# Kernel optimization log

Measured on AMD Instinct MI355X. Metric: run time of the kernel, lower is better.

## Reference

```python
import jax, jax.numpy as jnp
import numpy as np

N, E = 50000, 800000
NODE_DIM, EDGE_DIM = 96, 64
IN_DIM = 2 * NODE_DIM + EDGE_DIM  # 256


def setup_inputs() -> dict:
    key = jax.random.key(0)
    k = jax.random.split(key, 7)
    h = jax.random.normal(k[0], (N, NODE_DIM), dtype=jnp.float32)
    edge_index = jax.random.randint(k[1], (2, E), 0, N, dtype=jnp.int64)
    edge_attr = jax.random.normal(k[2], (E, EDGE_DIM), dtype=jnp.float32)
    # Linear params (PyTorch default-ish scale)
    s = 1.0 / np.sqrt(IN_DIM)
    W_e = jax.random.uniform(k[3], (IN_DIM, NODE_DIM), jnp.float32, -s, s)
    b_e = jax.random.uniform(k[4], (NODE_DIM,), jnp.float32, -s, s)
    W_n = jax.random.uniform(k[5], (IN_DIM, NODE_DIM), jnp.float32, -s, s)
    b_n = jax.random.uniform(k[6], (NODE_DIM,), jnp.float32, -s, s)
    return {"h": h, "edge_index": edge_index, "edge_attr": edge_attr,
            "W_e": W_e, "b_e": b_e, "W_n": W_n, "b_n": b_n}


def reference(h, edge_index, edge_attr, W_e, b_e, W_n, b_n):
    src, dst = edge_index[0], edge_index[1]
    concat = jnp.concatenate([h[src], h[dst], edge_attr], axis=-1)  # [E, 256]
    gates = jax.nn.sigmoid(concat @ W_e + b_e)                      # [E, node_dim]
    messages = jax.nn.softplus(concat @ W_n + b_n)                  # [E, node_dim]
    gated = gates * messages
    n = h.shape[0]
    h_new = jax.ops.segment_sum(gated, dst, num_segments=n)         # [N, node_dim]
    edge_count = jax.ops.segment_sum(jnp.ones((dst.shape[0],), h.dtype), dst, num_segments=n)
    edge_count = jnp.clip(edge_count, 1.0, None)[:, None]
    return h + h_new / edge_count
```

## Files before the change

kernel.cpp:

```cpp
#include <hip/hip_runtime.h>
#include <hip/hip_bf16.h>


#define NODE_DIM 96
#define EDGE_DIM 64
#define IN_DIM   256
#define NT_TILES 12
#define KT_TILES 8

typedef float  f32x4  __attribute__((ext_vector_type(4)));
typedef __bf16 bf16x8 __attribute__((ext_vector_type(8)));

__device__ __forceinline__ unsigned short bf16rne(float f) {
    unsigned int u = __float_as_uint(f);
    u += 0x7FFFu + ((u >> 16) & 1u);
    return (unsigned short)(u >> 16);
}

__global__ void pack_w_kernel(const float* __restrict__ We,
                              const float* __restrict__ Wn,
                              unsigned short* __restrict__ bpack) {
    int t = blockIdx.x * blockDim.x + threadIdx.x;
    if (t >= KT_TILES * NT_TILES * 64) return;
    int tile = t >> 6, lane = t & 63;
    int kt = tile / NT_TILES, nt = tile % NT_TILES;
    const float* W = (nt < 6) ? We : Wn;
    int n  = (nt % 6) * 16 + (lane & 15);
    int k0 = kt * 32 + (lane >> 4) * 8;
    union { unsigned short u[8]; uint4 v; } tmp;
#pragma unroll
    for (int j = 0; j < 8; ++j) tmp.u[j] = bf16rne(W[(k0 + j) * NODE_DIM + n]);
    *(uint4*)(bpack + (size_t)t * 8) = tmp.v;
}

__global__ void cvt_h_kernel(const float* __restrict__ h,
                             unsigned short* __restrict__ hb, int total8) {
    int i = blockIdx.x * 256 + threadIdx.x;
    if (i >= total8) return;
    const float4 v0 = ((const float4*)h)[i * 2];
    const float4 v1 = ((const float4*)h)[i * 2 + 1];
    union { unsigned short u[8]; uint4 v; } p;
    p.u[0] = bf16rne(v0.x); p.u[1] = bf16rne(v0.y);
    p.u[2] = bf16rne(v0.z); p.u[3] = bf16rne(v0.w);
    p.u[4] = bf16rne(v1.x); p.u[5] = bf16rne(v1.y);
    p.u[6] = bf16rne(v1.z); p.u[7] = bf16rne(v1.w);
    ((uint4*)hb)[i] = p.v;
}

__global__ void hist_kernel(const int* __restrict__ eidx, unsigned* __restrict__ deg, int E) {
    int e = blockIdx.x * 256 + threadIdx.x;
    if (e < E) atomicAdd(deg + eidx[E + e], 1u);
}

__device__ __forceinline__ unsigned block_excl_scan_256(unsigned v, int tid,
                                                        unsigned* wsum, unsigned* wpre,
                                                        unsigned* total) {
    int lane = tid & 63, w = tid >> 6;
    unsigned inc = v;
#pragma unroll
    for (int o = 1; o < 64; o <<= 1) {
        unsigned t = __shfl_up(inc, o, 64);
        if (lane >= o) inc += t;
    }
    if (lane == 63) wsum[w] = inc;
    __syncthreads();
    if (tid == 0) {
        unsigned s = 0;
#pragma unroll
        for (int k = 0; k < 4; ++k) { wpre[k] = s; s += wsum[k]; }
        *total = s;
    }
    __syncthreads();
    return inc - v + wpre[w];
}

__global__ void scan_block_kernel(const unsigned* __restrict__ deg,
                                  unsigned* __restrict__ scanned,
                                  unsigned* __restrict__ blocksum, int N) {
    __shared__ unsigned wsum[4], wpre[4], total;
    int tid = threadIdx.x;
    int i = blockIdx.x * 256 + tid;
    unsigned v = (i < N) ? deg[i] : 0u;
    unsigned excl = block_excl_scan_256(v, tid, wsum, wpre, &total);
    if (i < N) scanned[i] = excl;
    if (tid == 0) blocksum[blockIdx.x] = total;
}

__global__ void scan_sums_kernel(const unsigned* __restrict__ blocksum,
                                 unsigned* __restrict__ blockpref, int NB) {
    __shared__ unsigned wsum[4], wpre[4], total;
    int tid = threadIdx.x;
    unsigned v = (tid < NB) ? blocksum[tid] : 0u;
    unsigned excl = block_excl_scan_256(v, tid, wsum, wpre, &total);
    if (tid < NB) blockpref[tid] = excl;
}

__global__ void scan_finalize_kernel(const unsigned* __restrict__ scanned,
                                     const unsigned* __restrict__ blockpref,
                                     unsigned* __restrict__ offsets,
                                     unsigned* __restrict__ cursor, int N, int E) {
    int i = blockIdx.x * 256 + threadIdx.x;
    if (i < N) {
        unsigned o = scanned[i] + blockpref[i >> 8];
        offsets[i] = o;
        cursor[i]  = o;
    }
    if (i == 0) offsets[N] = (unsigned)E;
}

__global__ void scatter_kernel(const int* __restrict__ eidx,
                               unsigned* __restrict__ cursor,
                               int2* __restrict__ s_se,
                               int*  __restrict__ s_d,
                               int E) {
    int e = blockIdx.x * 256 + threadIdx.x;
    if (e < E) {
        int s = eidx[e];
        int d = eidx[E + e];
        unsigned pos = atomicAdd(cursor + d, 1u);
        s_se[pos] = make_int2(s, e);
        s_d[pos]  = d;
    }
}

__global__ __launch_bounds__(256, 3)
void gemm_sorted_kernel(const unsigned short* __restrict__ hb,
                        const int2* __restrict__ s_se,
                        const int*  __restrict__ s_d,
                        const float* __restrict__ ea,
                        const unsigned short* __restrict__ bpack,
                        const float* __restrict__ be,
                        const float* __restrict__ bn,
                        float* __restrict__ hnew,
                        int E) {
    const int tid  = threadIdx.x;
    const int wave = tid >> 6, lane = tid & 63;
    const int m    = lane & 15;
    const int quad = lane >> 4;
    const int base = blockIdx.x * 128 + wave * 32;

    const unsigned short* hsq[2];
    const unsigned short* hdq[2];
    const float*          epq[2];
    int dstv[2];
#pragma unroll
    for (int mt = 0; mt < 2; ++mt) {
        int r  = base + mt * 16 + m;
        int rg = (r < E) ? r : (E - 1);
        int2 se = s_se[rg];
        int dst = s_d[rg];
        dstv[mt] = dst;
        hsq[mt] = hb + (size_t)se.x * NODE_DIM + quad * 8;
        hdq[mt] = hb + (size_t)dst  * NODE_DIM + quad * 8;
        epq[mt] = ea + (size_t)se.y * EDGE_DIM + quad * 8;
    }
    const unsigned short* bl = bpack + lane * 8;

    f32x4 acc[2][NT_TILES];
#pragma unroll
    for (int mt = 0; mt < 2; ++mt)
#pragma unroll
        for (int nt = 0; nt < NT_TILES; ++nt) acc[mt][nt] = (f32x4){0.f, 0.f, 0.f, 0.f};

#pragma unroll
    for (int kt = 0; kt < KT_TILES; ++kt) {
        bf16x8 A[2];
#pragma unroll
        for (int mt = 0; mt < 2; ++mt) {
            if (kt < 3) {
                A[mt] = *(const bf16x8*)(hsq[mt] + kt * 32);
            } else if (kt < 6) {
                A[mt] = *(const bf16x8*)(hdq[mt] + (kt - 3) * 32);
            } else {
                const float4 v0 = *(const float4*)(epq[mt] + (kt - 6) * 32);
                const float4 v1 = *(const float4*)(epq[mt] + (kt - 6) * 32 + 4);
                union { unsigned short u[8]; bf16x8 b; } t;
                t.u[0] = bf16rne(v0.x); t.u[1] = bf16rne(v0.y);
                t.u[2] = bf16rne(v0.z); t.u[3] = bf16rne(v0.w);
                t.u[4] = bf16rne(v1.x); t.u[5] = bf16rne(v1.y);
                t.u[6] = bf16rne(v1.z); t.u[7] = bf16rne(v1.w);
                A[mt] = t.b;
            }
        }
#pragma unroll
        for (int nt = 0; nt < NT_TILES; ++nt) {
            bf16x8 bfrag = *(const bf16x8*)(bl + (kt * NT_TILES + nt) * 512);
            acc[0][nt] = __builtin_amdgcn_mfma_f32_16x16x32_bf16(A[0], bfrag, acc[0][nt], 0, 0, 0);
            acc[1][nt] = __builtin_amdgcn_mfma_f32_16x16x32_bf16(A[1], bfrag, acc[1][nt], 0, 0, 0);
        }
    }

#pragma unroll
    for (int mt = 0; mt < 2; ++mt) {
        int dprev = -1;
        float s[6];
#pragma unroll
        for (int r = 0; r < 4; ++r) {
            const int ee = base + mt * 16 + quad * 4 + r;
            const int d  = __shfl(dstv[mt], quad * 4 + r, 64);
            if (ee >= E) continue;
            float v[6];
#pragma unroll
            for (int nt = 0; nt < 6; ++nt) {
                const int col = nt * 16 + m;
                float g  = acc[mt][nt][r]     + be[col];
                float mm = acc[mt][nt + 6][r] + bn[col];
                float gate = 1.0f / (1.0f + __expf(-g));
                float sp   = fmaxf(mm, 0.0f) + __logf(1.0f + __expf(-fabsf(mm)));
                v[nt] = gate * sp;
            }
            if (d != dprev) {
                if (dprev >= 0) {
                    float* hrow = hnew + (size_t)dprev * NODE_DIM + m;
#pragma unroll
                    for (int nt = 0; nt < 6; ++nt) unsafeAtomicAdd(hrow + nt * 16, s[nt]);
                }
#pragma unroll
                for (int nt = 0; nt < 6; ++nt) s[nt] = v[nt];
                dprev = d;
            } else {
#pragma unroll
                for (int nt = 0; nt < 6; ++nt) s[nt] += v[nt];
            }
        }
        if (dprev >= 0) {
            float* hrow = hnew + (size_t)dprev * NODE_DIM + m;
#pragma unroll
            for (int nt = 0; nt < 6; ++nt) unsafeAtomicAdd(hrow + nt * 16, s[nt]);
        }
    }
}

__global__ void finalize_kernel(const float* __restrict__ h,
                                const float* __restrict__ hnew,
                                const unsigned* __restrict__ offsets,
                                float* __restrict__ out,
                                int total4) {
    int i = blockIdx.x * blockDim.x + threadIdx.x;
    if (i >= total4) return;
    int n = i / 24;
    unsigned deg = offsets[n + 1] - offsets[n];
    float inv = 1.0f / (float)(deg > 0u ? deg : 1u);
    float4 hv = ((const float4*)h)[i];
    float4 av = ((const float4*)hnew)[i];
    float4 o = {hv.x + av.x * inv, hv.y + av.y * inv, hv.z + av.z * inv, hv.w + av.w * inv};
    ((float4*)out)[i] = o;
}

extern "C" void kernel_launch(void* const* d_in, const int* in_sizes, int n_in,
                              void* d_out, int out_size, void* d_ws, size_t ws_size,
                              hipStream_t stream) {
    const float* h   = (const float*)d_in[0];
    const int*   ei  = (const int*)  d_in[1];
    const float* ea  = (const float*)d_in[2];
    const float* We  = (const float*)d_in[3];
    const float* be  = (const float*)d_in[4];
    const float* Wn  = (const float*)d_in[5];
    const float* bn  = (const float*)d_in[6];

    const int N = in_sizes[0] / NODE_DIM;
    const int E = in_sizes[2] / EDGE_DIM;
    char* ws = (char*)d_ws;

    size_t off = 0;
    auto take = [&](size_t bytes) { size_t o = off; off = (off + bytes + 511) & ~(size_t)511; return o; };
    const size_t O_BPACK = take((size_t)KT_TILES * NT_TILES * 64 * 16);
    const size_t O_DEG   = take((size_t)N * 4);
    const size_t O_HNEW  = take((size_t)N * NODE_DIM * 4);
    const size_t O_MEMSET_END = off;
    const size_t O_SCAN  = take((size_t)N * 4);
    const size_t O_BSUM  = take(1024);
    const size_t O_BPREF = take(1024);
    const size_t O_OFFS  = take((size_t)(N + 1) * 4);
    const size_t O_CURS  = take((size_t)N * 4);
    const size_t O_SSE   = take((size_t)E * 8);
    const size_t O_SD    = take((size_t)E * 4);
    const size_t O_HB    = take((size_t)N * NODE_DIM * 2);
    (void)ws_size;

    unsigned short* bpack = (unsigned short*)(ws + O_BPACK);
    unsigned* deg   = (unsigned*)(ws + O_DEG);
    float*    hnew  = (float*)(ws + O_HNEW);
    unsigned* scn   = (unsigned*)(ws + O_SCAN);
    unsigned* bsum  = (unsigned*)(ws + O_BSUM);
    unsigned* bpref = (unsigned*)(ws + O_BPREF);
    unsigned* offs  = (unsigned*)(ws + O_OFFS);
    unsigned* curs  = (unsigned*)(ws + O_CURS);
    int2*     s_se  = (int2*)(ws + O_SSE);
    int*      s_d   = (int*)(ws + O_SD);
    unsigned short* hb = (unsigned short*)(ws + O_HB);

    hipMemsetAsync(ws + O_DEG, 0, O_MEMSET_END - O_DEG, stream);

    pack_w_kernel<<<(KT_TILES * NT_TILES * 64 + 255) / 256, 256, 0, stream>>>(We, Wn, bpack);

    const int total8 = N * NODE_DIM / 8;
    cvt_h_kernel<<<(total8 + 255) / 256, 256, 0, stream>>>(h, hb, total8);

    const int NB = (N + 255) / 256;
    hist_kernel<<<(E + 255) / 256, 256, 0, stream>>>(ei, deg, E);
    scan_block_kernel<<<NB, 256, 0, stream>>>(deg, scn, bsum, N);
    scan_sums_kernel<<<1, 256, 0, stream>>>(bsum, bpref, NB);
    scan_finalize_kernel<<<NB, 256, 0, stream>>>(scn, bpref, offs, curs, N, E);
    scatter_kernel<<<(E + 255) / 256, 256, 0, stream>>>(ei, curs, s_se, s_d, E);

    gemm_sorted_kernel<<<(E + 127) / 128, 256, 0, stream>>>(hb, s_se, s_d, ea, bpack,
                                                            be, bn, hnew, E);

    const int total4 = N * (NODE_DIM / 4);
    finalize_kernel<<<(total4 + 255) / 256, 256, 0, stream>>>(h, hnew, offs, (float*)d_out, total4);
}
```

Baseline: 645.7 us.

## Fuse setup kernels, single-block scan, pre-sort bf16 edge attrs, two tiles per wave

Merges weight packing, h conversion and the degree histogram into one launch, and replaces the three-kernel scan with a single 1024-thread block scan. The scatter kernel now converts edge_attr to bf16 and writes it in dst-sorted order, so the GEMM reads contiguous bf16 rows instead of gathering fp32 rows by original edge index. The GEMM processes two 32-row tiles per wave, loading all A fragments up front and prefetching the second tile before the first epilogue. Occupancy hint drops from 3 to 2 blocks, and bias values are hoisted into registers. The trade-off is that the single-block scan serialises over N and the scatter kernel takes on extra write traffic.

```diff
diff --git a/kernel.cpp b/kernel.cpp
--- a/kernel.cpp
+++ b/kernel.cpp
@@ -4,9 +4,9 @@
 
 #define NODE_DIM 96
 #define EDGE_DIM 64
-#define IN_DIM   256
 #define NT_TILES 12
 #define KT_TILES 8
+#define PACK_BLOCKS 24
 
 typedef float  f32x4  __attribute__((ext_vector_type(4)));
 typedef __bf16 bf16x8 __attribute__((ext_vector_type(8)));
@@ -17,117 +17,120 @@
     return (unsigned short)(u >> 16);
 }
 
-__global__ void pack_w_kernel(const float* __restrict__ We,
-                              const float* __restrict__ Wn,
-                              unsigned short* __restrict__ bpack) {
-    int t = blockIdx.x * blockDim.x + threadIdx.x;
-    if (t >= KT_TILES * NT_TILES * 64) return;
-    int tile = t >> 6, lane = t & 63;
-    int kt = tile / NT_TILES, nt = tile % NT_TILES;
-    const float* W = (nt < 6) ? We : Wn;
-    int n  = (nt % 6) * 16 + (lane & 15);
-    int k0 = kt * 32 + (lane >> 4) * 8;
-    union { unsigned short u[8]; uint4 v; } tmp;
-#pragma unroll
-    for (int j = 0; j < 8; ++j) tmp.u[j] = bf16rne(W[(k0 + j) * NODE_DIM + n]);
-    *(uint4*)(bpack + (size_t)t * 8) = tmp.v;
-}
-
-__global__ void cvt_h_kernel(const float* __restrict__ h,
-                             unsigned short* __restrict__ hb, int total8) {
-    int i = blockIdx.x * 256 + threadIdx.x;
-    if (i >= total8) return;
-    const float4 v0 = ((const float4*)h)[i * 2];
-    const float4 v1 = ((const float4*)h)[i * 2 + 1];
-    union { unsigned short u[8]; uint4 v; } p;
-    p.u[0] = bf16rne(v0.x); p.u[1] = bf16rne(v0.y);
-    p.u[2] = bf16rne(v0.z); p.u[3] = bf16rne(v0.w);
-    p.u[4] = bf16rne(v1.x); p.u[5] = bf16rne(v1.y);
-    p.u[6] = bf16rne(v1.z); p.u[7] = bf16rne(v1.w);
-    ((uint4*)hb)[i] = p.v;
-}
-
-__global__ void hist_kernel(const int* __restrict__ eidx, unsigned* __restrict__ deg, int E) {
-    int e = blockIdx.x * 256 + threadIdx.x;
-    if (e < E) atomicAdd(deg + eidx[E + e], 1u);
-}
-
-__device__ __forceinline__ unsigned block_excl_scan_256(unsigned v, int tid,
-                                                        unsigned* wsum, unsigned* wpre,
-                                                        unsigned* total) {
-    int lane = tid & 63, w = tid >> 6;
-    unsigned inc = v;
-#pragma unroll
-    for (int o = 1; o < 64; o <<= 1) {
-        unsigned t = __shfl_up(inc, o, 64);
-        if (lane >= o) inc += t;
+__global__ __launch_bounds__(256)
+void setup_kernel(const float* __restrict__ We, const float* __restrict__ Wn,
+                  unsigned short* __restrict__ bpack,
+                  const float* __restrict__ h, unsigned short* __restrict__ hb,
+                  int total8,
+                  const int* __restrict__ eidx, unsigned* __restrict__ deg,
+                  int E, int cvtB) {
+    const int b = blockIdx.x, tid = threadIdx.x;
+    if (b < PACK_BLOCKS) {
+        int t = b * 256 + tid;
+        if (t < KT_TILES * NT_TILES * 64) {
+            int tile = t >> 6, lane = t & 63;
+            int kt = tile / NT_TILES, nt = tile % NT_TILES;
+            const float* W = (nt < 6) ? We : Wn;
+            int n  = (nt % 6) * 16 + (lane & 15);
+            int k0 = kt * 32 + (lane >> 4) * 8;
+            union { unsigned short u[8]; uint4 v; } tmp;
+#pragma unroll
+            for (int j = 0; j < 8; ++j) tmp.u[j] = bf16rne(W[(k0 + j) * NODE_DIM + n]);
+            *(uint4*)(bpack + (size_t)t * 8) = tmp.v;
+        }
+    } else if (b < PACK_BLOCKS + cvtB) {
+        int i = (b - PACK_BLOCKS) * 256 + tid;
+        if (i < total8) {
+            const float4 v0 = ((const float4*)h)[i * 2];
+            const float4 v1 = ((const float4*)h)[i * 2 + 1];
+            union { unsigned short u[8]; uint4 v; } p;
+            p.u[0] = bf16rne(v0.x); p.u[1] = bf16rne(v0.y);
+            p.u[2] = bf16rne(v0.z); p.u[3] = bf16rne(v0.w);
+            p.u[4] = bf16rne(v1.x); p.u[5] = bf16rne(v1.y);
+            p.u[6] = bf16rne(v1.z); p.u[7] = bf16rne(v1.w);
+            ((uint4*)hb)[i] = p.v;
+        }
+    } else {
+        int e = (b - PACK_BLOCKS - cvtB) * 256 + tid;
+        if (e < E) atomicAdd(deg + eidx[E + e], 1u);
     }
-    if (lane == 63) wsum[w] = inc;
-    __syncthreads();
-    if (tid == 0) {
-        unsigned s = 0;
-#pragma unroll
-        for (int k = 0; k < 4; ++k) { wpre[k] = s; s += wsum[k]; }
-        *total = s;
+}
+
+__global__ __launch_bounds__(1024)
+void scan_kernel(const unsigned* __restrict__ deg,
+                 unsigned* __restrict__ offsets,
+                 unsigned* __restrict__ cursor, int N) {
+    __shared__ unsigned lds_w[16], lds_p[16], lds_tot;
+    const int tid = threadIdx.x, lane = tid & 63, wv = tid >> 6;
+    unsigned carry = 0;
+    for (int base = 0; base < N; base += 1024) {
+        int i = base + tid;
+        unsigned v = (i < N) ? deg[i] : 0u;
+        unsigned inc = v;
+#pragma unroll
+        for (int o = 1; o < 64; o <<= 1) {
+            unsigned t = __shfl_up(inc, o, 64);
+            if (lane >= o) inc += t;
+        }
+        if (lane == 63) lds_w[wv] = inc;
+        __syncthreads();
+        if (tid == 0) {
+            unsigned s = 0;
+#pragma unroll
+            for (int k = 0; k < 16; ++k) { unsigned x = lds_w[k]; lds_p[k] = s; s += x; }
+            lds_tot = s;
+        }
+        __syncthreads();
+        unsigned excl = inc - v + lds_p[wv] + carry;
+        if (i < N) { offsets[i] = excl; cursor[i] = excl; }
+        carry += lds_tot;
+        __syncthreads();
     }
-    __syncthreads();
-    return inc - v + wpre[w];
-}
-
-__global__ void scan_block_kernel(const unsigned* __restrict__ deg,
-                                  unsigned* __restrict__ scanned,
-                                  unsigned* __restrict__ blocksum, int N) {
-    __shared__ unsigned wsum[4], wpre[4], total;
-    int tid = threadIdx.x;
-    int i = blockIdx.x * 256 + tid;
-    unsigned v = (i < N) ? deg[i] : 0u;
-    unsigned excl = block_excl_scan_256(v, tid, wsum, wpre, &total);
-    if (i < N) scanned[i] = excl;
-    if (tid == 0) blocksum[blockIdx.x] = total;
-}
-
-__global__ void scan_sums_kernel(const unsigned* __restrict__ blocksum,
-                                 unsigned* __restrict__ blockpref, int NB) {
-    __shared__ unsigned wsum[4], wpre[4], total;
-    int tid = threadIdx.x;
-    unsigned v = (tid < NB) ? blocksum[tid] : 0u;
-    unsigned excl = block_excl_scan_256(v, tid, wsum, wpre, &total);
-    if (tid < NB) blockpref[tid] = excl;
-}
-
-__global__ void scan_finalize_kernel(const unsigned* __restrict__ scanned,
-                                     const unsigned* __restrict__ blockpref,
-                                     unsigned* __restrict__ offsets,
-                                     unsigned* __restrict__ cursor, int N, int E) {
-    int i = blockIdx.x * 256 + threadIdx.x;
-    if (i < N) {
-        unsigned o = scanned[i] + blockpref[i >> 8];
-        offsets[i] = o;
-        cursor[i]  = o;
+    if (tid == 0) offsets[N] = carry;
+}
+
+__global__ __launch_bounds__(256)
+void scatter_kernel(const int* __restrict__ eidx, const float* __restrict__ ea,
+                    unsigned* __restrict__ cursor,
+                    int2* __restrict__ s_sd, unsigned short* __restrict__ seab,
+                    int E) {
+    const int tid = threadIdx.x, wave = tid >> 6, lane = tid & 63;
+    const int ebase = blockIdx.x * 256 + wave * 64;
+    const int e = ebase + lane;
+    unsigned pos = 0u;
+    if (e < E) {
+        int s = eidx[e], d = eidx[E + e];
+        pos = atomicAdd(cursor + d, 1u);
+        s_sd[pos] = make_int2(s, d);
     }
-    if (i == 0) offsets[N] = (unsigned)E;
-}
-
-__global__ void scatter_kernel(const int* __restrict__ eidx,
-                               unsigned* __restrict__ cursor,
-                               int2* __restrict__ s_se,
-                               int*  __restrict__ s_d,
-                               int E) {
-    int e = blockIdx.x * 256 + threadIdx.x;
-    if (e < E) {
-        int s = eidx[e];
-        int d = eidx[E + e];
-        unsigned pos = atomicAdd(cursor + d, 1u);
-        s_se[pos] = make_int2(s, e);
-        s_d[pos]  = d;
+#pragma unroll
+    for (int ph = 0; ph < 4; ++ph) {
+        const int el = ph * 16 + (lane >> 2);
+        const int q  = lane & 3;
+        const unsigned p = (unsigned)__shfl((int)pos, el, 64);
+        const int eo = ebase + el;
+        if (eo < E) {
+            const float4* pr = (const float4*)(ea + (size_t)eo * EDGE_DIM) + q * 4;
+            const float4 v0 = pr[0], v1 = pr[1], v2 = pr[2], v3 = pr[3];
+            union { unsigned short u[16]; uint4 v[2]; } t;
+            t.u[0]  = bf16rne(v0.x); t.u[1]  = bf16rne(v0.y);
+            t.u[2]  = bf16rne(v0.z); t.u[3]  = bf16rne(v0.w);
+            t.u[4]  = bf16rne(v1.x); t.u[5]  = bf16rne(v1.y);
+            t.u[6]  = bf16rne(v1.z); t.u[7]  = bf16rne(v1.w);
+            t.u[8]  = bf16rne(v2.x); t.u[9]  = bf16rne(v2.y);
+            t.u[10] = bf16rne(v2.z); t.u[11] = bf16rne(v2.w);
+            t.u[12] = bf16rne(v3.x); t.u[13] = bf16rne(v3.y);
+            t.u[14] = bf16rne(v3.z); t.u[15] = bf16rne(v3.w);
+            uint4* dp = (uint4*)(seab + (size_t)p * EDGE_DIM + q * 16);
+            dp[0] = t.v[0]; dp[1] = t.v[1];
+        }
     }
 }
 
-__global__ __launch_bounds__(256, 3)
+__global__ __launch_bounds__(256, 2)
 void gemm_sorted_kernel(const unsigned short* __restrict__ hb,
-                        const int2* __restrict__ s_se,
-                        const int*  __restrict__ s_d,
-                        const float* __restrict__ ea,
+                        const int2* __restrict__ s_sd,
+                        const unsigned short* __restrict__ seab,
                         const unsigned short* __restrict__ bpack,
                         const float* __restrict__ be,
                         const float* __restrict__ bn,
@@ -137,98 +140,112 @@
     const int wave = tid >> 6, lane = tid & 63;
     const int m    = lane & 15;
     const int quad = lane >> 4;
-    const int base = blockIdx.x * 128 + wave * 32;
-
-    const unsigned short* hsq[2];
-    const unsigned short* hdq[2];
-    const float*          epq[2];
-    int dstv[2];
-#pragma unroll
-    for (int mt = 0; mt < 2; ++mt) {
-        int r  = base + mt * 16 + m;
-        int rg = (r < E) ? r : (E - 1);
-        int2 se = s_se[rg];
-        int dst = s_d[rg];
-        dstv[mt] = dst;
-        hsq[mt] = hb + (size_t)se.x * NODE_DIM + quad * 8;
-        hdq[mt] = hb + (size_t)dst  * NODE_DIM + quad * 8;
-        epq[mt] = ea + (size_t)se.y * EDGE_DIM + quad * 8;
-    }
+    const int wbase = (blockIdx.x * 4 + wave) * 64;
+
     const unsigned short* bl = bpack + lane * 8;
 
+    float bev[6], bnv[6];
+#pragma unroll
+    for (int nt = 0; nt < 6; ++nt) { bev[nt] = be[nt * 16 + m]; bnv[nt] = bn[nt * 16 + m]; }
+
+    int2 sd[2][2];
+#pragma unroll
+    for (int T = 0; T < 2; ++T)
+#pragma unroll
+        for (int mt = 0; mt < 2; ++mt) {
+            int r  = wbase + T * 32 + mt * 16 + m;
+            int rg = (r < E) ? r : (E - 1);
+            sd[T][mt] = s_sd[rg];
+        }
+
+    bf16x8 a[2][8];
     f32x4 acc[2][NT_TILES];
-#pragma unroll
-    for (int mt = 0; mt < 2; ++mt)
-#pragma unroll
-        for (int nt = 0; nt < NT_TILES; ++nt) acc[mt][nt] = (f32x4){0.f, 0.f, 0.f, 0.f};
-
-#pragma unroll
-    for (int kt = 0; kt < KT_TILES; ++kt) {
-        bf16x8 A[2];
+
+    auto load_a = [&](int T) {
 #pragma unroll
         for (int mt = 0; mt < 2; ++mt) {
-            if (kt < 3) {
-                A[mt] = *(const bf16x8*)(hsq[mt] + kt * 32);
-            } else if (kt < 6) {
-                A[mt] = *(const bf16x8*)(hdq[mt] + (kt - 3) * 32);
-            } else {
-                const float4 v0 = *(const float4*)(epq[mt] + (kt - 6) * 32);
-                const float4 v1 = *(const float4*)(epq[mt] + (kt - 6) * 32 + 4);
-                union { unsigned short u[8]; bf16x8 b; } t;
-                t.u[0] = bf16rne(v0.x); t.u[1] = bf16rne(v0.y);
-                t.u[2] = bf16rne(v0.z); t.u[3] = bf16rne(v0.w);
-                t.u[4] = bf16rne(v1.x); t.u[5] = bf16rne(v1.y);
-                t.u[6] = bf16rne(v1.z); t.u[7] = bf16rne(v1.w);
-                A[mt] = t.b;
+            int r  = wbase + T * 32 + mt * 16 + m;
+            int rg = (r < E) ? r : (E - 1);
+            const unsigned short* hs = hb + (size_t)sd[T][mt].x * NODE_DIM + quad * 8;
+            const unsigned short* hd = hb + (size_t)sd[T][mt].y * NODE_DIM + quad * 8;
+            const unsigned short* ep = seab + (size_t)rg * EDGE_DIM + quad * 8;
+#pragma unroll
+            for (int kt = 0; kt < 3; ++kt) a[mt][kt]     = *(const bf16x8*)(hs + kt * 32);
+#pragma unroll
+            for (int kt = 0; kt < 3; ++kt) a[mt][3 + kt] = *(const bf16x8*)(hd + kt * 32);
+            a[mt][6] = *(const bf16x8*)(ep);
+            a[mt][7] = *(const bf16x8*)(ep + 32);
+        }
+    };
+
+    auto zero_acc = [&]() {
+#pragma unroll
+        for (int mt = 0; mt < 2; ++mt)
+#pragma unroll
+            for (int nt = 0; nt < NT_TILES; ++nt) acc[mt][nt] = (f32x4){0.f, 0.f, 0.f, 0.f};
+    };
+
+    auto mfma_all = [&]() {
+#pragma unroll
+        for (int kt = 0; kt < KT_TILES; ++kt) {
+#pragma unroll
+            for (int nt = 0; nt < NT_TILES; ++nt) {
+                bf16x8 bfrag = *(const bf16x8*)(bl + (kt * NT_TILES + nt) * 512);
+                acc[0][nt] = __builtin_amdgcn_mfma_f32_16x16x32_bf16(a[0][kt], bfrag, acc[0][nt], 0, 0, 0);
+                acc[1][nt] = __builtin_amdgcn_mfma_f32_16x16x32_bf16(a[1][kt], bfrag, acc[1][nt], 0, 0, 0);
             }
         }
-#pragma unroll
-        for (int nt = 0; nt < NT_TILES; ++nt) {
-            bf16x8 bfrag = *(const bf16x8*)(bl + (kt * NT_TILES + nt) * 512);
-            acc[0][nt] = __builtin_amdgcn_mfma_f32_16x16x32_bf16(A[0], bfrag, acc[0][nt], 0, 0, 0);
-            acc[1][nt] = __builtin_amdgcn_mfma_f32_16x16x32_bf16(A[1], bfrag, acc[1][nt], 0, 0, 0);
-        }
-    }
-
-#pragma unroll
-    for (int mt = 0; mt < 2; ++mt) {
-        int dprev = -1;
-        float s[6];
-#pragma unroll
-        for (int r = 0; r < 4; ++r) {
-            const int ee = base + mt * 16 + quad * 4 + r;
-            const int d  = __shfl(dstv[mt], quad * 4 + r, 64);
-            if (ee >= E) continue;
-            float v[6];
-#pragma unroll
-            for (int nt = 0; nt < 6; ++nt) {
-                const int col = nt * 16 + m;
-                float g  = acc[mt][nt][r]     + be[col];
-                float mm = acc[mt][nt + 6][r] + bn[col];
-                float gate = 1.0f / (1.0f + __expf(-g));
-                float sp   = fmaxf(mm, 0.0f) + __logf(1.0f + __expf(-fabsf(mm)));
-                v[nt] = gate * sp;
+    };
+
+    auto epilogue = [&](int T) {
+#pragma unroll
+        for (int mt = 0; mt < 2; ++mt) {
+            int dprev = -1;
+            float s[6];
+#pragma unroll
+            for (int r = 0; r < 4; ++r) {
+                const int ee = wbase + T * 32 + mt * 16 + quad * 4 + r;
+                const int d  = __shfl(sd[T][mt].y, quad * 4 + r, 64);
+                if (ee >= E) continue;
+                float v[6];
+#pragma unroll
+                for (int nt = 0; nt < 6; ++nt) {
+                    float g  = acc[mt][nt][r]     + bev[nt];
+                    float mm = acc[mt][nt + 6][r] + bnv[nt];
+                    float gate = 1.0f / (1.0f + __expf(-g));
+                    float sp   = fmaxf(mm, 0.0f) + __logf(1.0f + __expf(-fabsf(mm)));
+                    v[nt] = gate * sp;
+                }
+                if (d != dprev) {
+                    if (dprev >= 0) {
+                        float* hrow = hnew + (size_t)dprev * NODE_DIM + m;
+#pragma unroll
+                        for (int nt = 0; nt < 6; ++nt) unsafeAtomicAdd(hrow + nt * 16, s[nt]);
+                    }
+#pragma unroll
+                    for (int nt = 0; nt < 6; ++nt) s[nt] = v[nt];
+                    dprev = d;
+                } else {
+#pragma unroll
+                    for (int nt = 0; nt < 6; ++nt) s[nt] += v[nt];
+                }
             }
-            if (d != dprev) {
-                if (dprev >= 0) {
-                    float* hrow = hnew + (size_t)dprev * NODE_DIM + m;
-#pragma unroll
-                    for (int nt = 0; nt < 6; ++nt) unsafeAtomicAdd(hrow + nt * 16, s[nt]);
-                }
-#pragma unroll
-                for (int nt = 0; nt < 6; ++nt) s[nt] = v[nt];
-                dprev = d;
-            } else {
-#pragma unroll
-                for (int nt = 0; nt < 6; ++nt) s[nt] += v[nt];
+            if (dprev >= 0) {
+                float* hrow = hnew + (size_t)dprev * NODE_DIM + m;
+#pragma unroll
+                for (int nt = 0; nt < 6; ++nt) unsafeAtomicAdd(hrow + nt * 16, s[nt]);
             }
         }
-        if (dprev >= 0) {
-            float* hrow = hnew + (size_t)dprev * NODE_DIM + m;
-#pragma unroll
-            for (int nt = 0; nt < 6; ++nt) unsafeAtomicAdd(hrow + nt * 16, s[nt]);
-        }
-    }
+    };
+
+    load_a(0);
+    zero_acc();
+    mfma_all();
+    load_a(1);
+    epilogue(0);
+    zero_acc();
+    mfma_all();
+    epilogue(1);
 }
 
 __global__ void finalize_kernel(const float* __restrict__ h,
@@ -268,43 +285,35 @@
     const size_t O_DEG   = take((size_t)N * 4);
     const size_t O_HNEW  = take((size_t)N * NODE_DIM * 4);
     const size_t O_MEMSET_END = off;
-    const size_t O_SCAN  = take((size_t)N * 4);
-    const size_t O_BSUM  = take(1024);
-    const size_t O_BPREF = take(1024);
     const size_t O_OFFS  = take((size_t)(N + 1) * 4);
     const size_t O_CURS  = take((size_t)N * 4);
-    const size_t O_SSE   = take((size_t)E * 8);
-    const size_t O_SD    = take((size_t)E * 4);
+    const size_t O_SSD   = take((size_t)E * 8);
+    const size_t O_SEAB  = take((size_t)E * EDGE_DIM * 2);
     const size_t O_HB    = take((size_t)N * NODE_DIM * 2);
     (void)ws_size;
 
     unsigned short* bpack = (unsigned short*)(ws + O_BPACK);
     unsigned* deg   = (unsigned*)(ws + O_DEG);
     float*    hnew  = (float*)(ws + O_HNEW);
-    unsigned* scn   = (unsigned*)(ws + O_SCAN);
-    unsigned* bsum  = (unsigned*)(ws + O_BSUM);
-    unsigned* bpref = (unsigned*)(ws + O_BPREF);
     unsigned* offs  = (unsigned*)(ws + O_OFFS);
     unsigned* curs  = (unsigned*)(ws + O_CURS);
-    int2*     s_se  = (int2*)(ws + O_SSE);
-    int*      s_d   = (int*)(ws + O_SD);
-    unsigned short* hb = (unsigned short*)(ws + O_HB);
+    int2*     s_sd  = (int2*)(ws + O_SSD);
+    unsigned short* seab = (unsigned short*)(ws + O_SEAB);
+    unsigned short* hb   = (unsigned short*)(ws + O_HB);
 
     hipMemsetAsync(ws + O_DEG, 0, O_MEMSET_END - O_DEG, stream);
 
-    pack_w_kernel<<<(KT_TILES * NT_TILES * 64 + 255) / 256, 256, 0, stream>>>(We, Wn, bpack);
-
     const int total8 = N * NODE_DIM / 8;
-    cvt_h_kernel<<<(total8 + 255) / 256, 256, 0, stream>>>(h, hb, total8);
-
-    const int NB = (N + 255) / 256;
-    hist_kernel<<<(E + 255) / 256, 256, 0, stream>>>(ei, deg, E);
-    scan_block_kernel<<<NB, 256, 0, stream>>>(deg, scn, bsum, N);
-    scan_sums_kernel<<<1, 256, 0, stream>>>(bsum, bpref, NB);
-    scan_finalize_kernel<<<NB, 256, 0, stream>>>(scn, bpref, offs, curs, N, E);
-    scatter_kernel<<<(E + 255) / 256, 256, 0, stream>>>(ei, curs, s_se, s_d, E);
-
-    gemm_sorted_kernel<<<(E + 127) / 128, 256, 0, stream>>>(hb, s_se, s_d, ea, bpack,
+    const int cvtB   = (total8 + 255) / 256;
+    const int histB  = (E + 255) / 256;
+    setup_kernel<<<PACK_BLOCKS + cvtB + histB, 256, 0, stream>>>(
+        We, Wn, bpack, h, hb, total8, ei, deg, E, cvtB);
+
+    scan_kernel<<<1, 1024, 0, stream>>>(deg, offs, curs, N);
+
+    scatter_kernel<<<(E + 255) / 256, 256, 0, stream>>>(ei, ea, curs, s_sd, seab, E);
+
+    gemm_sorted_kernel<<<(E + 255) / 256, 256, 0, stream>>>(hb, s_sd, seab, bpack,
                                                             be, bn, hnew, E);
 
     const int total4 = N * (NODE_DIM / 4);
```

After: 980.9 us. 51.9% more time.
